# Optimization experiments

Measured on AMD Instinct MI355X. Metric: run time of the kernel, lower is better.

## Reference

```python
import jax, jax.numpy as jnp
import numpy as np

RADIUS = 0.2
NUM_POINTS = 32
MAX_POINTS = 60
BN_EPS = 1e-5


def _bn(x, g, b, m, v):
    # BatchNorm in eval mode (running stats), channels-last broadcast
    return g * (x - m) * jax.lax.rsqrt(v + BN_EPS) + b


def setup_inputs() -> dict:
    key = jax.random.key(0)
    nk = lambda i: jax.random.fold_in(key, i)
    B, NQ, NC, HC = 2, 4096, 8192, 64
    inp = {}
    inp['p_query'] = jax.random.uniform(nk(0), (B, NQ, 3), dtype=jnp.float32)
    inp['p_context'] = jax.random.uniform(nk(1), (B, NC, 3), dtype=jnp.float32)
    inp['h_context'] = jax.random.normal(nk(2), (B, NC, HC), dtype=jnp.float32)

    def lin(i, o, ci):
        return (jax.random.normal(nk(i), (o, ci), jnp.float32) / np.sqrt(ci).astype(np.float32),
                0.01 * jax.random.normal(nk(i + 1), (o,), jnp.float32))

    def bnp(i, c):
        return (1.0 + 0.1 * jax.random.normal(nk(i), (c,), jnp.float32),
                0.1 * jax.random.normal(nk(i + 1), (c,), jnp.float32),
                0.1 * jax.random.normal(nk(i + 2), (c,), jnp.float32),
                0.5 + jax.random.uniform(nk(i + 3), (c,), jnp.float32))

    inp['w_xyz'], inp['b_xyz'] = lin(10, 64, 3)
    # pointwise 1x1 Conv2d MLP: 128 -> 128 -> 128 -> 256 (BN after each conv)
    inp['pw_w1'], inp['pw_b1'] = lin(12, 128, 128)
    inp['pw_g1'], inp['pw_be1'], inp['pw_m1'], inp['pw_v1'] = bnp(14, 128)
    inp['pw_w2'], inp['pw_b2'] = lin(20, 128, 128)
    inp['pw_g2'], inp['pw_be2'], inp['pw_m2'], inp['pw_v2'] = bnp(22, 128)
    inp['pw_w3'], inp['pw_b3'] = lin(28, 256, 128)
    inp['pw_g3'], inp['pw_be3'], inp['pw_m3'], inp['pw_v3'] = bnp(30, 256)
    # global 1x1 Conv1d MLP: 256 -> 128 -> 64 -> 3 (BN+ReLU between, none on last)
    inp['g_w1'], inp['g_b1'] = lin(36, 128, 256)
    inp['g_g1'], inp['g_be1'], inp['g_m1'], inp['g_v1'] = bnp(38, 128)
    inp['g_w2'], inp['g_b2'] = lin(44, 64, 128)
    inp['g_g2'], inp['g_be2'], inp['g_m2'], inp['g_v2'] = bnp(46, 64)
    inp['g_w3'], inp['g_b3'] = lin(52, 3, 64)
    return inp


def reference(p_query, p_context, h_context, w_xyz, b_xyz,
              pw_w1, pw_b1, pw_g1, pw_be1, pw_m1, pw_v1,
              pw_w2, pw_b2, pw_g2, pw_be2, pw_m2, pw_v2,
              pw_w3, pw_b3, pw_g3, pw_be3, pw_m3, pw_v3,
              g_w1, g_b1, g_g1, g_be1, g_m1, g_v1,
              g_w2, g_b2, g_g2, g_be2, g_m2, g_v2,
              g_w3, g_b3):
    N = p_context.shape[1]
    # knn_points: squared distances, K smallest sorted ascending
    d = (jnp.sum(p_query ** 2, -1)[:, :, None]
         - 2.0 * jnp.einsum('bqd,bnd->bqn', p_query, p_context)
         + jnp.sum(p_context ** 2, -1)[:, None, :])  # [B,NQ,NC]
    neg, idx = jax.lax.top_k(-d, MAX_POINTS)
    dist = -neg  # [B,NQ,K] ascending
    knn_idx = jnp.where(dist > RADIUS ** 2, N + 1, idx)
    idx = knn_idx[:, :, :NUM_POINTS]
    dist = dist[:, :, :NUM_POINTS]
    mask = idx == N + 1
    idx = jnp.where(mask, 0, idx)
    dist = jnp.where(mask, 0.0, dist)
    gather = jax.vmap(lambda a, i: a[i])
    pts = gather(p_context, idx)        # [B,NQ,P,3]
    h_group = gather(h_context, idx)    # [B,NQ,P,HC]
    p_rel = pts - p_query[:, :, None, :]
    h_rel = p_rel @ w_xyz.T + b_xyz     # Linear(3 -> 64)
    h = jnp.concatenate([h_rel, h_group], -1)  # [B,NQ,P,128]
    h = jax.nn.relu(_bn(h @ pw_w1.T + pw_b1, pw_g1, pw_be1, pw_m1, pw_v1))
    h = jax.nn.relu(_bn(h @ pw_w2.T + pw_b2, pw_g2, pw_be2, pw_m2, pw_v2))
    h = _bn(h @ pw_w3.T + pw_b3, pw_g3, pw_be3, pw_m3, pw_v3)  # [B,NQ,P,256]
    # cosine radius weighting (note: dist is SQUARED distance, faithful to source)
    c = 0.5 * (jnp.cos(dist * (np.pi / RADIUS)) + 1.0)
    c = jnp.where((dist <= RADIUS) & (dist > 0.0), c, 0.0)
    y = jnp.sum(h * c[..., None], axis=2)  # masked weighted pool over neighbors -> [B,NQ,256]
    y = jax.nn.relu(_bn(y @ g_w1.T + g_b1, g_g1, g_be1, g_m1, g_v1))
    y = jax.nn.relu(_bn(y @ g_w2.T + g_b2, g_g2, g_be2, g_m2, g_v2))
    return y @ g_w3.T + g_b3  # [B,NQ,3]
```

## Files before the change

kernel.cpp:

```cpp
#include <hip/hip_runtime.h>
#include <hip/hip_bf16.h>
#include <math.h>

#define BB 2
#define NQ 4096
#define NC 8192
#define KNN 32
#define WCAP 512
#define BN_EPS 1e-5f

typedef __attribute__((ext_vector_type(8))) short s16x8;
typedef __attribute__((ext_vector_type(4))) float f32x4;

#define WS_IDX   0
#define WS_CW    1048576
#define WS_Z     2097152
#define WS_SQ    6291456
#define WS_PCF   6324224
#define WS_PIDX  6586368
#define WS_CELL  6651904
#define WS_CCNT  6717440
#define WS_COFS  6718464
#define WS_W1    6719488
#define WS_W2    6752256
#define WS_W3    6785024
#define WS_GW1   6850560
#define WS_GW2   6916096
#define WS_F3    6932480
#define WS_FG1   6934528
#define WS_FG2   6935552
#define WS_FD1   6936064
#define WS_FD2   6937088

__device__ inline int swz(int row, int kbyte, int rb) {
    return row * rb + (kbyte ^ ((row & 7) << 4));
}
__device__ inline unsigned short f2bf(float x) {
    __hip_bfloat16 h = __float2bfloat16(x);
    return *reinterpret_cast<unsigned short*>(&h);
}
__device__ inline float bf2f(unsigned short u) {
    return __uint_as_float(((unsigned)u) << 16);
}
__device__ inline int cell1d(float x) {
    int c = (int)floorf(x * 5.0f);
    return c < 0 ? 0 : (c > 4 ? 4 : c);
}

__device__ inline void mk_img(const float* __restrict__ src, int R, int K, char* dst, int t, int NT)
{
    int rbg = (K * 2) / 16;
    int ng = R * rbg;
    for (int g = t; g < ng; g += NT) {
        int row = g / rbg;
        int b16 = (g - row * rbg) * 16;
        int sb  = b16 ^ ((row & 7) << 4);
        const float* s = src + row * K + sb / 2;
        union { s16x8 v; unsigned short u[8]; } pk;
#pragma unroll
        for (int j = 0; j < 8; ++j) pk.u[j] = f2bf(s[j]);
        *(s16x8*)(dst + row * (K * 2) + b16) = pk.v;
    }
}

__global__ __launch_bounds__(256) void prep_kernel(
    const float* __restrict__ pc,
    const float* __restrict__ w1, const float* __restrict__ w2, const float* __restrict__ w3,
    const float* __restrict__ gw1, const float* __restrict__ gw2,
    const float* __restrict__ b1, const float* __restrict__ g1, const float* __restrict__ m1,
    const float* __restrict__ v1, const float* __restrict__ be1,
    const float* __restrict__ b2, const float* __restrict__ g2, const float* __restrict__ m2,
    const float* __restrict__ v2, const float* __restrict__ be2,
    const float* __restrict__ g3, const float* __restrict__ b3, const float* __restrict__ m3,
    const float* __restrict__ v3, const float* __restrict__ be3,
    const float* __restrict__ gg1, const float* __restrict__ gb1, const float* __restrict__ gm1,
    const float* __restrict__ gv1, const float* __restrict__ gbe1,
    const float* __restrict__ gg2, const float* __restrict__ gb2, const float* __restrict__ gm2,
    const float* __restrict__ gv2, const float* __restrict__ gbe2,
    char* __restrict__ ws)
{
    const int t = blockIdx.x * 256 + threadIdx.x;
    const int NT = gridDim.x * 256;

    int* cell = (int*)(ws + WS_CELL);
    int* ccnt = (int*)(ws + WS_CCNT);
    for (int i = t; i < BB * NC; i += NT) {
        float x = pc[i*3+0], y = pc[i*3+1], z = pc[i*3+2];
        int c = (cell1d(z)*5 + cell1d(y))*5 + cell1d(x);
        cell[i] = c;
        atomicAdd(&ccnt[(i >> 13)*128 + c], 1);
    }

    mk_img(w1,  128, 128, ws + WS_W1,  t, NT);
    mk_img(w2,  128, 128, ws + WS_W2,  t, NT);
    mk_img(w3,  256, 128, ws + WS_W3,  t, NT);
    mk_img(gw1, 128, 256, ws + WS_GW1, t, NT);
    mk_img(gw2,  64, 128, ws + WS_GW2, t, NT);

    if (t < 256) {
        float s = g3[t] * rsqrtf(v3[t] + BN_EPS);
        ((float2*)(ws + WS_F3))[t] = make_float2(s, s * (b3[t] - m3[t]) + be3[t]);
    }
    if (t < 128) {
        float s = gg1[t] * rsqrtf(gv1[t] + BN_EPS);
        ((float2*)(ws + WS_FG1))[t] = make_float2(s, s * (gb1[t] - gm1[t]) + gbe1[t]);
        float s0 = g1[t] * rsqrtf(v1[t] + BN_EPS);
        ((float2*)(ws + WS_FD1))[t] = make_float2(s0, s0 * (b1[t] - m1[t]) + be1[t]);
        float s1 = g2[t] * rsqrtf(v2[t] + BN_EPS);
        ((float2*)(ws + WS_FD2))[t] = make_float2(s1, s1 * (b2[t] - m2[t]) + be2[t]);
    }
    if (t < 64) {
        float s = gg2[t] * rsqrtf(gv2[t] + BN_EPS);
        ((float2*)(ws + WS_FG2))[t] = make_float2(s, s * (gb2[t] - gm2[t]) + gbe2[t]);
    }
}

__global__ __launch_bounds__(128) void scan_kernel(char* __restrict__ ws)
{
    int* ccnt = (int*)(ws + WS_CCNT);
    int* cofs = (int*)(ws + WS_COFS);
    const int wv = threadIdx.x >> 6, lane = threadIdx.x & 63;
    const int base = wv * 128;
    int a = (lane < 125) ? ccnt[base + lane] : 0;
    int b = (64 + lane < 125) ? ccnt[base + 64 + lane] : 0;
    int ai = a, bi = b;
    for (int d = 1; d < 64; d <<= 1) {
        int t = __shfl_up(ai, d, 64);
        if (lane >= d) ai += t;
    }
    int totA = __shfl(ai, 63, 64);
    for (int d = 1; d < 64; d <<= 1) {
        int t = __shfl_up(bi, d, 64);
        if (lane >= d) bi += t;
    }
    int exA = ai - a;
    int exB = totA + bi - b;
    cofs[base + lane] = exA;       cofs[base + 64 + lane] = exB;
    ccnt[base + lane] = exA;       ccnt[base + 64 + lane] = exB;
}

__global__ __launch_bounds__(256) void scatter_kernel(
    const float* __restrict__ pc, char* __restrict__ ws)
{
    const int i = blockIdx.x * 256 + threadIdx.x;
    if (i >= BB * NC) return;
    const int b = i >> 13, loc = i & (NC - 1);
    int* cell = (int*)(ws + WS_CELL);
    int* cur  = (int*)(ws + WS_CCNT);
    float4* pcf = (float4*)(ws + WS_PCF);
    int*    pidx = (int*)(ws + WS_PIDX);
    int c = cell[i];
    int pos = atomicAdd(&cur[b*128 + c], 1);
    float x = pc[i*3+0], y = pc[i*3+1], z = pc[i*3+2];
    float w = (x*x + y*y) + z*z;
    pcf[(size_t)b*NC + pos]  = make_float4(x, y, z, w);
    pidx[(size_t)b*NC + pos] = loc;
}

__device__ inline void cmpxu(unsigned long long& k, int j, bool up) {
    unsigned long long ok = __shfl_xor(k, j, 64);
    bool lower = ((threadIdx.x & 63) & j) == 0;
    bool take = (lower == up) ? (k > ok) : (k < ok);
    if (take) k = ok;
}
__device__ inline void sortasc64(unsigned long long& k) {
    const int lane = threadIdx.x & 63;
    for (int kk = 2; kk <= 64; kk <<= 1)
        for (int j = kk >> 1; j > 0; j >>= 1)
            cmpxu(k, j, (lane & kk) == 0);
}
__device__ inline void sortdesc64(unsigned long long& k) {
    const int lane = threadIdx.x & 63;
    for (int kk = 2; kk <= 64; kk <<= 1)
        for (int j = kk >> 1; j > 0; j >>= 1)
            cmpxu(k, j, (lane & kk) != 0);
}
__device__ inline void merge128(unsigned long long& k0, unsigned long long& k1) {
    if (k0 > k1) { unsigned long long t = k0; k0 = k1; k1 = t; }
#pragma unroll
    for (int j = 32; j > 0; j >>= 1) { cmpxu(k0, j, true); cmpxu(k1, j, true); }
}
__device__ inline void cmpx64(unsigned long long& k, int& p, int j, bool up) {
    unsigned long long ok = __shfl_xor(k, j, 64);
    int op = __shfl_xor(p, j, 64);
    bool lower = ((threadIdx.x & 63) & j) == 0;
    bool gt = (k > ok) || (k == ok && p > op);
    bool take = (lower == up) ? gt : !gt;
    if (take) { k = ok; p = op; }
}
__device__ inline void sortasc64kp(unsigned long long& k, int& p) {
    const int lane = threadIdx.x & 63;
    for (int kk = 2; kk <= 64; kk <<= 1)
        for (int j = kk >> 1; j > 0; j >>= 1)
            cmpx64(k, p, j, (lane & kk) == 0);
}

__global__ __launch_bounds__(256) void knn_kernel(
    const float* __restrict__ pq, const float* __restrict__ pc,
    const float4* __restrict__ pcf, const int* __restrict__ pidx,
    const int* __restrict__ cofs,
    int* __restrict__ idx_out, float* __restrict__ cw_out)
{
    __shared__ unsigned long long kbuf[4][WCAP];

    const int tid = threadIdx.x, lane = tid & 63, w = tid >> 6;
    const int gq = blockIdx.x * 4 + w;
    const int b = gq >> 12;

    const float qxf = pq[gq*3+0], qyf = pq[gq*3+1], qzf = pq[gq*3+2];
    const double qx = (double)qxf, qy = (double)qyf, qz = (double)qzf;
    const double sq = qx*qx + qy*qy + qz*qz;
    const float  sqf = (float)sq;
    const double R2d = 0.2 * 0.2;
    const float  R2f = 0.04f + 1e-4f;

    const float4* pcfb = pcf + (size_t)b * NC;
    const int*    pidb = pidx + (size_t)b * NC;
    const int*    cb   = cofs + b * 128;
    const float*  pcb  = pc + (size_t)b * NC * 3;

    int xlo = (int)floorf((qxf - 0.2f) * 5.0f - 1e-3f); xlo = xlo < 0 ? 0 : xlo;
    int xhi = (int)floorf((qxf + 0.2f) * 5.0f + 1e-3f); xhi = xhi > 4 ? 4 : xhi;
    int ylo = (int)floorf((qyf - 0.2f) * 5.0f - 1e-3f); ylo = ylo < 0 ? 0 : ylo;
    int yhi = (int)floorf((qyf + 0.2f) * 5.0f + 1e-3f); yhi = yhi > 4 ? 4 : yhi;
    int zlo = (int)floorf((qzf - 0.2f) * 5.0f - 1e-3f); zlo = zlo < 0 ? 0 : zlo;
    int zhi = (int)floorf((qzf + 0.2f) * 5.0f + 1e-3f); zhi = zhi > 4 ? 4 : zhi;

    const unsigned long long lt = (lane == 63) ? ~0ULL >> 1 : (1ULL << lane) - 1;
    int cnt = 0;
    for (int zi = zlo; zi <= zhi; ++zi) {
        for (int yi = ylo; yi <= yhi; ++yi) {
            int row = (zi*5 + yi)*5;
            int s = cb[row + xlo], e = cb[row + xhi + 1];
            for (int t0 = s; t0 < e; t0 += 64) {
                int t = t0 + lane;
                bool pred = false;
                unsigned long long key = ~0ULL;
                if (t < e) {
                    float4 cd = pcfb[t];
                    float dot = (qxf*cd.x + qyf*cd.y) + qzf*cd.z;
                    float d   = (sqf - 2.0f*dot) + cd.w;
                    pred = (d <= R2f);
                    if (pred) {
                        float dc = fmaxf(d, 0.0f);
                        key = ((unsigned long long)__float_as_uint(dc) << 32)
                            | (unsigned)pidb[t];
                    }
                }
                unsigned long long mask = __ballot(pred);
                if (pred) {
                    int pos = cnt + __popcll(mask & lt);
                    if (pos < WCAP) kbuf[w][pos] = key;
                }
                cnt += __popcll(mask);
            }
        }
    }
    if (cnt > WCAP) cnt = WCAP;

    unsigned long long k0 = (lane < cnt)      ? kbuf[w][lane]      : ~0ULL;
    unsigned long long k1 = (64 + lane < cnt) ? kbuf[w][64 + lane] : ~0ULL;
    sortasc64(k0);
    sortdesc64(k1);
    merge128(k0, k1);
    int consumed = 128;
    while (consumed < cnt) {
        int i1 = consumed + lane;
        k1 = (i1 < cnt) ? kbuf[w][i1] : ~0ULL;
        sortdesc64(k1);
        merge128(k0, k1);
        consumed += 64;
    }

    unsigned long long kf = ~0ULL;
    int pf = 0x7fffffff;
    if (k0 != ~0ULL) {
        int n = (int)(k0 & 0xffffffffULL);
        double cx = (double)pcb[n*3+0];
        double cy = (double)pcb[n*3+1];
        double cz = (double)pcb[n*3+2];
        double dot = qx*cx + qy*cy + qz*cz;
        double sc  = cx*cx + cy*cy + cz*cz;
        double d   = (sq - 2.0*dot) + sc;
        if (d <= R2d) {
            double dc = d < 0.0 ? 0.0 : d;
            kf = (unsigned long long)__double_as_longlong(dc);
            pf = n;
        }
    }
    sortasc64kp(kf, pf);

    if (lane < KNN) {
        int id = 0; float c = 0.0f;
        if (kf != ~0ULL) {
            id = pf;
            double d = __longlong_as_double((long long)kf);
            if (d > 0.0 && d <= 0.2) {
                double cw = 0.5 * (cos(d * 15.707963267948966) + 1.0);
                c = (float)cw;
            }
        }
        idx_out[gq*KNN + lane] = id;
        cw_out[gq*KNN + lane]  = c;
    }
}

__global__ __launch_bounds__(256, 2) void front_kernel(
    const float* __restrict__ pq, const float* __restrict__ pc, const float* __restrict__ hc,
    const float* __restrict__ w_xyz, const float* __restrict__ b_xyz,
    const char* __restrict__ w1img, const char* __restrict__ w2img,
    const float2* __restrict__ fd1, const float2* __restrict__ fd2,
    const int* __restrict__ idx_in, const float* __restrict__ cw_in,
    float* __restrict__ z_buf, float* __restrict__ sq_buf)
{
    __shared__ __align__(16) char smem[35840];
    const int tid = threadIdx.x, lane = tid & 63, w = tid >> 6;
    char*  slice = smem + w * 8960;
    int*   Sidx  = (int*)  (slice + 8192);
    float* Cwl   = (float*)(slice + 8320);
    float* Prel  = (float*)(slice + 8448);

    const int gq = blockIdx.x * 4 + w;
    const int b = gq >> 12;
    const float* pcb = pc + (size_t)b * NC * 3;
    const float* hcb = hc + (size_t)b * NC * 64;

    float cwv = 0.0f;
    if (lane < 32) {
        int id = idx_in[gq*KNN + lane];
        cwv = cw_in[gq*KNN + lane];
        Sidx[lane] = id;
        Cwl[lane]  = cwv;
        Prel[lane*3+0] = pcb[id*3+0] - pq[gq*3+0];
        Prel[lane*3+1] = pcb[id*3+1] - pq[gq*3+1];
        Prel[lane*3+2] = pcb[id*3+2] - pq[gq*3+2];
    }
    {
        float sv = cwv;
        sv += __shfl_xor(sv, 1, 64);
        sv += __shfl_xor(sv, 2, 64);
        sv += __shfl_xor(sv, 4, 64);
        sv += __shfl_xor(sv, 8, 64);
        sv += __shfl_xor(sv, 16, 64);
        if (lane == 0) sq_buf[gq] = sv;
    }

#pragma unroll 1
    for (int it = 0; it < 8; ++it) {
        int p = it*64 + lane;
        int row = p >> 4, seg = p & 15;
        float vals[8];
        if (seg >= 8) {
            const float* src = hcb + (size_t)Sidx[row]*64 + (seg-8)*8;
            float4 u0 = *(const float4*)src;
            float4 u1 = *(const float4*)(src+4);
            vals[0]=u0.x; vals[1]=u0.y; vals[2]=u0.z; vals[3]=u0.w;
            vals[4]=u1.x; vals[5]=u1.y; vals[6]=u1.z; vals[7]=u1.w;
        } else {
            float px = Prel[row*3+0], py = Prel[row*3+1], pz = Prel[row*3+2];
            int c0 = seg*8;
#pragma unroll
            for (int j = 0; j < 8; ++j) {
                int c = c0 + j;
                vals[j] = px*w_xyz[c*3+0] + py*w_xyz[c*3+1] + pz*w_xyz[c*3+2] + b_xyz[c];
            }
        }
        union { s16x8 v; unsigned short u[8]; } pk;
#pragma unroll
        for (int j = 0; j < 8; ++j) pk.u[j] = f2bf(vals[j]);
        *(s16x8*)(slice + swz(row, seg*16, 256)) = pk.v;
    }

    const int cl = lane & 15, q4 = lane >> 4;

    {
        f32x4 acc[2][8];
#pragma unroll
        for (int m = 0; m < 2; ++m)
#pragma unroll
            for (int nt = 0; nt < 8; ++nt) acc[m][nt] = (f32x4){0.f,0.f,0.f,0.f};
#pragma unroll
        for (int kk = 0; kk < 4; ++kk) {
            int kbyte = kk*64 + q4*16;
            s16x8 a0 = *(const s16x8*)(slice + swz(cl,      kbyte, 256));
            s16x8 a1 = *(const s16x8*)(slice + swz(16 + cl, kbyte, 256));
#pragma unroll
            for (int nt = 0; nt < 8; ++nt) {
                s16x8 bwv = *(const s16x8*)(w1img + swz(nt*16 + cl, kbyte, 256));
                acc[0][nt] = __builtin_amdgcn_mfma_f32_16x16x32_bf16(a0, bwv, acc[0][nt], 0, 0, 0);
                acc[1][nt] = __builtin_amdgcn_mfma_f32_16x16x32_bf16(a1, bwv, acc[1][nt], 0, 0, 0);
            }
        }
#pragma unroll
        for (int nt = 0; nt < 8; ++nt) {
            int j = nt*16 + cl;
            float2 f = fd1[j];
#pragma unroll
            for (int m = 0; m < 2; ++m)
#pragma unroll
                for (int r = 0; r < 4; ++r) {
                    int row = m*16 + q4*4 + r;
                    float x = fmaxf(acc[m][nt][r]*f.x + f.y, 0.0f);
                    unsigned int me = f2bf(x);
                    unsigned int ot = (unsigned int)__shfl_xor((int)me, 1, 64);
                    if ((cl & 1) == 0) {
                        *(unsigned int*)(slice + swz(row, j*2, 256)) = me | (ot << 16);
                    }
                }
        }
    }

    {
        f32x4 acc[2][8];
#pragma unroll
        for (int m = 0; m < 2; ++m)
#pragma unroll
            for (int nt = 0; nt < 8; ++nt) acc[m][nt] = (f32x4){0.f,0.f,0.f,0.f};
#pragma unroll
        for (int kk = 0; kk < 4; ++kk) {
            int kbyte = kk*64 + q4*16;
            s16x8 a0 = *(const s16x8*)(slice + swz(cl,      kbyte, 256));
            s16x8 a1 = *(const s16x8*)(slice + swz(16 + cl, kbyte, 256));
#pragma unroll
            for (int nt = 0; nt < 8; ++nt) {
                s16x8 bwv = *(const s16x8*)(w2img + swz(nt*16 + cl, kbyte, 256));
                acc[0][nt] = __builtin_amdgcn_mfma_f32_16x16x32_bf16(a0, bwv, acc[0][nt], 0, 0, 0);
                acc[1][nt] = __builtin_amdgcn_mfma_f32_16x16x32_bf16(a1, bwv, acc[1][nt], 0, 0, 0);
            }
        }
        float cwr[2][4];
#pragma unroll
        for (int m = 0; m < 2; ++m)
#pragma unroll
            for (int r = 0; r < 4; ++r) cwr[m][r] = Cwl[m*16 + q4*4 + r];
#pragma unroll
        for (int nt = 0; nt < 8; ++nt) {
            int j = nt*16 + cl;
            float2 f = fd2[j];
            float sum = 0.0f;
#pragma unroll
            for (int m = 0; m < 2; ++m)
#pragma unroll
                for (int r = 0; r < 4; ++r) {
                    float x = fmaxf(acc[m][nt][r]*f.x + f.y, 0.0f);
                    sum += cwr[m][r] * x;
                }
            sum += __shfl_xor(sum, 16, 64);
            sum += __shfl_xor(sum, 32, 64);
            if (q4 == 0) z_buf[(size_t)gq*128 + j] = sum;
        }
    }
}

__global__ __launch_bounds__(256) void tail_kernel(
    const char* __restrict__ w3img, const char* __restrict__ gw1img, const char* __restrict__ gw2img,
    const float2* __restrict__ f3, const float2* __restrict__ fg1, const float2* __restrict__ fg2,
    const float* __restrict__ z_buf, const float* __restrict__ sq_buf,
    const float* __restrict__ gw3, const float* __restrict__ gb3,
    float* __restrict__ out)
{
    __shared__ __align__(16) char smem[123136];
    char* A1 = smem;
    char* A2 = smem + 16384;
    char* A4 = smem + 49152;
    char* Wb = smem + 57344;
    float* Ssm = (float*)(smem + 122880);

    const int tid = threadIdx.x;
    const int q0 = blockIdx.x * 64;

    for (int g = tid; g < 1024; g += 256) {
        int row = g >> 4, seg = g & 15;
        const float* zs = z_buf + (size_t)(q0 + row)*128 + seg*8;
        float4 u0 = *(const float4*)zs;
        float4 u1 = *(const float4*)(zs+4);
        union { s16x8 v; unsigned short u[8]; } pk;
        pk.u[0]=f2bf(u0.x); pk.u[1]=f2bf(u0.y); pk.u[2]=f2bf(u0.z); pk.u[3]=f2bf(u0.w);
        pk.u[4]=f2bf(u1.x); pk.u[5]=f2bf(u1.y); pk.u[6]=f2bf(u1.z); pk.u[7]=f2bf(u1.w);
        *(s16x8*)(A1 + swz(row, seg*16, 256)) = pk.v;
    }
    for (int p = tid; p < 4096; p += 256) ((s16x8*)Wb)[p] = ((const s16x8*)w3img)[p];
    if (tid < 64) Ssm[tid] = sq_buf[q0 + tid];
    __syncthreads();

    const int l = tid & 63, w = tid >> 6;
    const int r0 = w*16, cl = l & 15, q4 = l >> 4;

    {
        f32x4 acc[16];
#pragma unroll
        for (int nt = 0; nt < 16; ++nt) acc[nt] = (f32x4){0.f,0.f,0.f,0.f};
#pragma unroll
        for (int kk = 0; kk < 4; ++kk) {
            int kbyte = kk*64 + q4*16;
            s16x8 a0 = *(const s16x8*)(A1 + swz(r0 + cl, kbyte, 256));
#pragma unroll
            for (int nt = 0; nt < 16; ++nt) {
                s16x8 bwv = *(const s16x8*)(Wb + swz(nt*16 + cl, kbyte, 256));
                acc[nt] = __builtin_amdgcn_mfma_f32_16x16x32_bf16(a0, bwv, acc[nt], 0, 0, 0);
            }
        }
#pragma unroll
        for (int nt = 0; nt < 16; ++nt) {
            int j = nt*16 + cl;
            float2 f = f3[j];
#pragma unroll
            for (int r = 0; r < 4; ++r) {
                int row = r0 + q4*4 + r;
                float S = Ssm[row];
                float x = f.x*acc[nt][r] + S*f.y;
                *(unsigned short*)(A2 + swz(row, j*2, 512)) = f2bf(x);
            }
        }
    }
    __syncthreads();
    for (int p = tid; p < 4096; p += 256) ((s16x8*)Wb)[p] = ((const s16x8*)gw1img)[p];
    __syncthreads();

    {
        f32x4 acc[8];
#pragma unroll
        for (int nt = 0; nt < 8; ++nt) acc[nt] = (f32x4){0.f,0.f,0.f,0.f};
#pragma unroll
        for (int kk = 0; kk < 8; ++kk) {
            int kbyte = kk*64 + q4*16;
            s16x8 a0 = *(const s16x8*)(A2 + swz(r0 + cl, kbyte, 512));
#pragma unroll
            for (int nt = 0; nt < 8; ++nt) {
                s16x8 bwv = *(const s16x8*)(Wb + swz(nt*16 + cl, kbyte, 512));
                acc[nt] = __builtin_amdgcn_mfma_f32_16x16x32_bf16(a0, bwv, acc[nt], 0, 0, 0);
            }
        }
#pragma unroll
        for (int nt = 0; nt < 8; ++nt) {
            int j = nt*16 + cl;
            float2 f = fg1[j];
#pragma unroll
            for (int r = 0; r < 4; ++r) {
                int row = r0 + q4*4 + r;
                float x = fmaxf(f.x*acc[nt][r] + f.y, 0.0f);
                *(unsigned short*)(A1 + swz(row, j*2, 256)) = f2bf(x);
            }
        }
    }
    __syncthreads();
    for (int p = tid; p < 1024; p += 256) ((s16x8*)Wb)[p] = ((const s16x8*)gw2img)[p];
    __syncthreads();

    {
        f32x4 acc[4];
#pragma unroll
        for (int nt = 0; nt < 4; ++nt) acc[nt] = (f32x4){0.f,0.f,0.f,0.f};
#pragma unroll
        for (int kk = 0; kk < 4; ++kk) {
            int kbyte = kk*64 + q4*16;
            s16x8 a0 = *(const s16x8*)(A1 + swz(r0 + cl, kbyte, 256));
#pragma unroll
            for (int nt = 0; nt < 4; ++nt) {
                s16x8 bwv = *(const s16x8*)(Wb + swz(nt*16 + cl, kbyte, 256));
                acc[nt] = __builtin_amdgcn_mfma_f32_16x16x32_bf16(a0, bwv, acc[nt], 0, 0, 0);
            }
        }
#pragma unroll
        for (int nt = 0; nt < 4; ++nt) {
            int j = nt*16 + cl;
            float2 f = fg2[j];
#pragma unroll
            for (int r = 0; r < 4; ++r) {
                int row = r0 + q4*4 + r;
                float x = fmaxf(f.x*acc[nt][r] + f.y, 0.0f);
                *(unsigned short*)(A4 + swz(row, j*2, 128)) = f2bf(x);
            }
        }
    }
    __syncthreads();

    if (tid < 192) {
        int q = tid / 3, jj = tid - q*3;
        const float* wr = gw3 + jj*64;
        float s = 0.0f;
        for (int k = 0; k < 64; ++k) {
            unsigned short u = *(const unsigned short*)(A4 + swz(q, k*2, 128));
            s += bf2f(u) * wr[k];
        }
        out[(size_t)(q0 + q)*3 + jj] = s + gb3[jj];
    }
}

extern "C" void kernel_launch(void* const* d_in, const int* in_sizes, int n_in,
                              void* d_out, int out_size, void* d_ws, size_t ws_size,
                              hipStream_t stream)
{
    const float* pq    = (const float*)d_in[0];
    const float* pc    = (const float*)d_in[1];
    const float* hc    = (const float*)d_in[2];
    const float* w_xyz = (const float*)d_in[3];
    const float* b_xyz = (const float*)d_in[4];
    const float* w1    = (const float*)d_in[5];
    const float* b1    = (const float*)d_in[6];
    const float* g1    = (const float*)d_in[7];
    const float* be1   = (const float*)d_in[8];
    const float* m1    = (const float*)d_in[9];
    const float* v1    = (const float*)d_in[10];
    const float* w2    = (const float*)d_in[11];
    const float* b2    = (const float*)d_in[12];
    const float* g2    = (const float*)d_in[13];
    const float* be2   = (const float*)d_in[14];
    const float* m2    = (const float*)d_in[15];
    const float* v2    = (const float*)d_in[16];
    const float* w3    = (const float*)d_in[17];
    const float* b3    = (const float*)d_in[18];
    const float* g3    = (const float*)d_in[19];
    const float* be3   = (const float*)d_in[20];
    const float* m3    = (const float*)d_in[21];
    const float* v3    = (const float*)d_in[22];
    const float* gw1   = (const float*)d_in[23];
    const float* gb1   = (const float*)d_in[24];
    const float* gg1   = (const float*)d_in[25];
    const float* gbe1  = (const float*)d_in[26];
    const float* gm1   = (const float*)d_in[27];
    const float* gv1   = (const float*)d_in[28];
    const float* gw2   = (const float*)d_in[29];
    const float* gb2   = (const float*)d_in[30];
    const float* gg2   = (const float*)d_in[31];
    const float* gbe2  = (const float*)d_in[32];
    const float* gm2   = (const float*)d_in[33];
    const float* gv2   = (const float*)d_in[34];
    const float* gw3   = (const float*)d_in[35];
    const float* gb3   = (const float*)d_in[36];

    char* ws = (char*)d_ws;
    int*   idx_buf = (int*)(ws + WS_IDX);
    float* cw_buf  = (float*)(ws + WS_CW);
    float* z_buf   = (float*)(ws + WS_Z);
    float* sq_buf  = (float*)(ws + WS_SQ);

    hipMemsetAsync(ws + WS_CCNT, 0, 1024, stream);

    prep_kernel<<<64, 256, 0, stream>>>(pc, w1, w2, w3, gw1, gw2,
        b1, g1, m1, v1, be1, b2, g2, m2, v2, be2,
        g3, b3, m3, v3, be3, gg1, gb1, gm1, gv1, gbe1, gg2, gb2, gm2, gv2, gbe2, ws);

    scan_kernel<<<1, 128, 0, stream>>>(ws);

    scatter_kernel<<<(BB*NC + 255)/256, 256, 0, stream>>>(pc, ws);

    knn_kernel<<<(BB*NQ)/4, 256, 0, stream>>>(pq, pc,
        (const float4*)(ws + WS_PCF), (const int*)(ws + WS_PIDX),
        (const int*)(ws + WS_COFS), idx_buf, cw_buf);

    front_kernel<<<(BB*NQ)/4, 256, 0, stream>>>(pq, pc, hc, w_xyz, b_xyz,
        ws + WS_W1, ws + WS_W2,
        (const float2*)(ws + WS_FD1), (const float2*)(ws + WS_FD2),
        idx_buf, cw_buf, z_buf, sq_buf);

    tail_kernel<<<(BB*NQ)/64, 256, 0, stream>>>(
        ws + WS_W3, ws + WS_GW1, ws + WS_GW2,
        (const float2*)(ws + WS_F3), (const float2*)(ws + WS_FG1), (const float2*)(ws + WS_FG2),
        z_buf, sq_buf, gw3, gb3, (float*)d_out);
}
```

Before: 165.1 us.

## Fuse KNN search into front MLP kernel and stage weights in LDS

Merges the KNN kernel and the front pointwise-MLP kernel into a single kernel. Neighbor indices and cosine weights now stay in shared memory instead of going through global workspace buffers, which also saves one launch. The W1 and W2 bf16 weight images are additionally copied into shared memory before each MFMA stage, so B operands are read from LDS rather than global/L1. The cost is a larger LDS footprint (~67KB per block), which may reduce occupancy, plus extra block-wide barriers. Waves with cheap KNN searches now wait at those barriers for waves with expensive ones.

```diff
diff --git a/kernel.cpp b/kernel.cpp
--- a/kernel.cpp
+++ b/kernel.cpp
@@ -12,8 +12,6 @@
 typedef __attribute__((ext_vector_type(8))) short s16x8;
 typedef __attribute__((ext_vector_type(4))) float f32x4;
 
-#define WS_IDX   0
-#define WS_CW    1048576
 #define WS_Z     2097152
 #define WS_SQ    6291456
 #define WS_PCF   6324224
@@ -195,17 +193,27 @@
             cmpx64(k, p, j, (lane & kk) == 0);
 }
 
-__global__ __launch_bounds__(256) void knn_kernel(
-    const float* __restrict__ pq, const float* __restrict__ pc,
-    const float4* __restrict__ pcf, const int* __restrict__ pidx,
-    const int* __restrict__ cofs,
-    int* __restrict__ idx_out, float* __restrict__ cw_out)
+__global__ __launch_bounds__(256, 2) void knn_front_kernel(
+    const float* __restrict__ pq, const float* __restrict__ pc, const float* __restrict__ hc,
+    const float* __restrict__ w_xyz, const float* __restrict__ b_xyz,
+    const float4* __restrict__ pcf, const int* __restrict__ pidx, const int* __restrict__ cofs,
+    const char* __restrict__ w1img, const char* __restrict__ w2img,
+    const float2* __restrict__ fd1, const float2* __restrict__ fd2,
+    float* __restrict__ z_buf, float* __restrict__ sq_buf)
 {
-    __shared__ unsigned long long kbuf[4][WCAP];
-
+    __shared__ __align__(16) char smem[68608];
     const int tid = threadIdx.x, lane = tid & 63, w = tid >> 6;
+    char*  slice = smem + w * 8960;
+    int*   Sidx  = (int*)  (slice + 8192);
+    float* Cwl   = (float*)(slice + 8320);
+    float* Prel  = (float*)(slice + 8448);
+    char*  Wb    = smem + 35840;
+    unsigned long long* kb = (unsigned long long*)(smem + 35840 + w * 4096);
+
     const int gq = blockIdx.x * 4 + w;
     const int b = gq >> 12;
+    const float* pcb = pc + (size_t)b * NC * 3;
+    const float* hcb = hc + (size_t)b * NC * 64;
 
     const float qxf = pq[gq*3+0], qyf = pq[gq*3+1], qzf = pq[gq*3+2];
     const double qx = (double)qxf, qy = (double)qyf, qz = (double)qzf;
@@ -217,7 +225,6 @@
     const float4* pcfb = pcf + (size_t)b * NC;
     const int*    pidb = pidx + (size_t)b * NC;
     const int*    cb   = cofs + b * 128;
-    const float*  pcb  = pc + (size_t)b * NC * 3;
 
     int xlo = (int)floorf((qxf - 0.2f) * 5.0f - 1e-3f); xlo = xlo < 0 ? 0 : xlo;
     int xhi = (int)floorf((qxf + 0.2f) * 5.0f + 1e-3f); xhi = xhi > 4 ? 4 : xhi;
@@ -250,7 +257,7 @@
                 unsigned long long mask = __ballot(pred);
                 if (pred) {
                     int pos = cnt + __popcll(mask & lt);
-                    if (pos < WCAP) kbuf[w][pos] = key;
+                    if (pos < WCAP) kb[pos] = key;
                 }
                 cnt += __popcll(mask);
             }
@@ -258,15 +265,15 @@
     }
     if (cnt > WCAP) cnt = WCAP;
 
-    unsigned long long k0 = (lane < cnt)      ? kbuf[w][lane]      : ~0ULL;
-    unsigned long long k1 = (64 + lane < cnt) ? kbuf[w][64 + lane] : ~0ULL;
+    unsigned long long k0 = (lane < cnt)      ? kb[lane]      : ~0ULL;
+    unsigned long long k1 = (64 + lane < cnt) ? kb[64 + lane] : ~0ULL;
     sortasc64(k0);
     sortdesc64(k1);
     merge128(k0, k1);
     int consumed = 128;
     while (consumed < cnt) {
         int i1 = consumed + lane;
-        k1 = (i1 < cnt) ? kbuf[w][i1] : ~0ULL;
+        k1 = (i1 < cnt) ? kb[i1] : ~0ULL;
         sortdesc64(k1);
         merge128(k0, k1);
         consumed += 64;
@@ -290,6 +297,7 @@
     }
     sortasc64kp(kf, pf);
 
+    float cwv = 0.0f;
     if (lane < KNN) {
         int id = 0; float c = 0.0f;
         if (kf != ~0ULL) {
@@ -300,40 +308,12 @@
                 c = (float)cw;
             }
         }
-        idx_out[gq*KNN + lane] = id;
-        cw_out[gq*KNN + lane]  = c;
-    }
-}
-
-__global__ __launch_bounds__(256, 2) void front_kernel(
-    const float* __restrict__ pq, const float* __restrict__ pc, const float* __restrict__ hc,
-    const float* __restrict__ w_xyz, const float* __restrict__ b_xyz,
-    const char* __restrict__ w1img, const char* __restrict__ w2img,
-    const float2* __restrict__ fd1, const float2* __restrict__ fd2,
-    const int* __restrict__ idx_in, const float* __restrict__ cw_in,
-    float* __restrict__ z_buf, float* __restrict__ sq_buf)
-{
-    __shared__ __align__(16) char smem[35840];
-    const int tid = threadIdx.x, lane = tid & 63, w = tid >> 6;
-    char*  slice = smem + w * 8960;
-    int*   Sidx  = (int*)  (slice + 8192);
-    float* Cwl   = (float*)(slice + 8320);
-    float* Prel  = (float*)(slice + 8448);
-
-    const int gq = blockIdx.x * 4 + w;
-    const int b = gq >> 12;
-    const float* pcb = pc + (size_t)b * NC * 3;
-    const float* hcb = hc + (size_t)b * NC * 64;
-
-    float cwv = 0.0f;
-    if (lane < 32) {
-        int id = idx_in[gq*KNN + lane];
-        cwv = cw_in[gq*KNN + lane];
+        cwv = c;
         Sidx[lane] = id;
-        Cwl[lane]  = cwv;
-        Prel[lane*3+0] = pcb[id*3+0] - pq[gq*3+0];
-        Prel[lane*3+1] = pcb[id*3+1] - pq[gq*3+1];
-        Prel[lane*3+2] = pcb[id*3+2] - pq[gq*3+2];
+        Cwl[lane]  = c;
+        Prel[lane*3+0] = pcb[id*3+0] - qxf;
+        Prel[lane*3+1] = pcb[id*3+1] - qyf;
+        Prel[lane*3+2] = pcb[id*3+2] - qzf;
     }
     {
         float sv = cwv;
@@ -371,6 +351,14 @@
         *(s16x8*)(slice + swz(row, seg*16, 256)) = pk.v;
     }
 
+    __syncthreads();
+    {
+        const s16x8* wimg = (const s16x8*)w1img;
+        s16x8* Wv = (s16x8*)Wb;
+        for (int p = tid; p < 2048; p += 256) Wv[p] = wimg[p];
+    }
+    __syncthreads();
+
     const int cl = lane & 15, q4 = lane >> 4;
 
     {
@@ -386,7 +374,7 @@
             s16x8 a1 = *(const s16x8*)(slice + swz(16 + cl, kbyte, 256));
 #pragma unroll
             for (int nt = 0; nt < 8; ++nt) {
-                s16x8 bwv = *(const s16x8*)(w1img + swz(nt*16 + cl, kbyte, 256));
+                s16x8 bwv = *(const s16x8*)(Wb + swz(nt*16 + cl, kbyte, 256));
                 acc[0][nt] = __builtin_amdgcn_mfma_f32_16x16x32_bf16(a0, bwv, acc[0][nt], 0, 0, 0);
                 acc[1][nt] = __builtin_amdgcn_mfma_f32_16x16x32_bf16(a1, bwv, acc[1][nt], 0, 0, 0);
             }
@@ -410,6 +398,14 @@
         }
     }
 
+    __syncthreads();
+    {
+        const s16x8* wimg = (const s16x8*)w2img;
+        s16x8* Wv = (s16x8*)Wb;
+        for (int p = tid; p < 2048; p += 256) Wv[p] = wimg[p];
+    }
+    __syncthreads();
+
     {
         f32x4 acc[2][8];
 #pragma unroll
@@ -423,7 +419,7 @@
             s16x8 a1 = *(const s16x8*)(slice + swz(16 + cl, kbyte, 256));
 #pragma unroll
             for (int nt = 0; nt < 8; ++nt) {
-                s16x8 bwv = *(const s16x8*)(w2img + swz(nt*16 + cl, kbyte, 256));
+                s16x8 bwv = *(const s16x8*)(Wb + swz(nt*16 + cl, kbyte, 256));
                 acc[0][nt] = __builtin_amdgcn_mfma_f32_16x16x32_bf16(a0, bwv, acc[0][nt], 0, 0, 0);
                 acc[1][nt] = __builtin_amdgcn_mfma_f32_16x16x32_bf16(a1, bwv, acc[1][nt], 0, 0, 0);
             }
@@ -630,8 +626,6 @@
     const float* gb3   = (const float*)d_in[36];
 
     char* ws = (char*)d_ws;
-    int*   idx_buf = (int*)(ws + WS_IDX);
-    float* cw_buf  = (float*)(ws + WS_CW);
     float* z_buf   = (float*)(ws + WS_Z);
     float* sq_buf  = (float*)(ws + WS_SQ);
 
@@ -645,14 +639,12 @@
 
     scatter_kernel<<<(BB*NC + 255)/256, 256, 0, stream>>>(pc, ws);
 
-    knn_kernel<<<(BB*NQ)/4, 256, 0, stream>>>(pq, pc,
+    knn_front_kernel<<<(BB*NQ)/4, 256, 0, stream>>>(pq, pc, hc, w_xyz, b_xyz,
         (const float4*)(ws + WS_PCF), (const int*)(ws + WS_PIDX),
-        (const int*)(ws + WS_COFS), idx_buf, cw_buf);
-
-    front_kernel<<<(BB*NQ)/4, 256, 0, stream>>>(pq, pc, hc, w_xyz, b_xyz,
+        (const int*)(ws + WS_COFS),
         ws + WS_W1, ws + WS_W2,
         (const float2*)(ws + WS_FD1), (const float2*)(ws + WS_FD2),
-        idx_buf, cw_buf, z_buf, sq_buf);
+        z_buf, sq_buf);
 
     tail_kernel<<<(BB*NQ)/64, 256, 0, stream>>>(
         ws + WS_W3, ws + WS_GW1, ws + WS_GW2,
```

Result: slower. 199.5 us (+20.8%).
